# Performance work log

Hardware: AMD Instinct MI355X
Metric: run time of the kernel (lower is better)

## Reference

```python
import jax, jax.numpy as jnp
import numpy as np


def _normalize(x, axis=-1, eps=1e-12):
    n = jnp.linalg.norm(x, axis=axis, keepdims=True)
    return x / jnp.maximum(n, eps)


def _mlp(x, w1, b1, w2, b2):
    return jnp.maximum(x @ w1 + b1, 0.0) @ w2 + b2


def _quat_mul(a, b):
    # openfold (w, x, y, z) convention, Hamilton product
    aw, ax, ay, az = a[..., 0], a[..., 1], a[..., 2], a[..., 3]
    bw, bx, by, bz = b[..., 0], b[..., 1], b[..., 2], b[..., 3]
    return jnp.stack([
        aw * bw - ax * bx - ay * by - az * bz,
        aw * bx + ax * bw + ay * bz - az * by,
        aw * by - ax * bz + ay * bw + az * bx,
        aw * bz + ax * by - ay * bx + az * bw], axis=-1)


def _quat_rotate(q, v):
    # rotate vector v by unit quaternion q
    w = q[..., :1]
    u = q[..., 1:]
    t = 2.0 * jnp.cross(u, v)
    return v + w * t + jnp.cross(u, t)


def _conj(q):
    return q * jnp.asarray([1.0, -1.0, -1.0, -1.0], dtype=q.dtype)


def setup_inputs() -> dict:
    B, N, P, H, E, M = 2, 384, 128, 64, 32, 64
    key = jax.random.key(0)
    ks = iter(jax.random.split(key, 64))

    def nrm(shape):
        return jax.random.normal(next(ks), shape, dtype=jnp.float32)

    inp = {
        "frames_q": _normalize(nrm((B, N, 4))),
        "frames_x": nrm((B, N, 3)),
        "torsions": nrm((B, N, 7, 2)),
        "h": nrm((B, N, H)),
        "e": nrm((B, N, N, E)),
        "node_mask": jnp.ones((B, N), dtype=bool),
        "pocket_h": nrm((B, P, H)),
        "pocket_e": nrm((B, N, P, E)),
        "pocket_q": _normalize(nrm((B, P, 4))),
        "pocket_x": nrm((B, P, 3)),
        "pocket_mask": jnp.ones((B, P), dtype=bool),
    }
    # 2-layer MLPs with transition_size = 64
    for name, (fin, fout) in {"msg": (2 * H + E + 9, M), "feat": (H + M, H),
                              "tr": (M, 3), "qu": (M, 4), "to": (M, 14)}.items():
        inp[f"{name}_w1"] = nrm((fin, 64)) / np.sqrt(fin)
        inp[f"{name}_b1"] = nrm((64,)) * 0.01
        inp[f"{name}_w2"] = nrm((64, fout)) / np.sqrt(64)
        inp[f"{name}_b2"] = nrm((fout,)) * 0.01
    return inp


def reference(frames_q, frames_x, torsions, h, e, node_mask, pocket_h, pocket_e,
              pocket_q, pocket_x, pocket_mask,
              msg_w1, msg_b1, msg_w2, msg_b2,
              feat_w1, feat_b1, feat_w2, feat_b2,
              tr_w1, tr_b1, tr_w2, tr_b2,
              qu_w1, qu_b1, qu_w2, qu_b2,
              to_w1, to_b1, to_w2, to_b2):
    B, N, Hd = h.shape
    P = pocket_h.shape[-2]

    q_all = jnp.concatenate([frames_q, pocket_q], axis=-2)  # [B, N+P, 4]
    x_all = jnp.concatenate([frames_x, pocket_x], axis=-2)  # [B, N+P, 3]

    eye = jnp.eye(N, dtype=bool)
    mm = jnp.concatenate([
        node_mask[:, :, None] & node_mask[:, None, :] & ~eye,
        node_mask[:, :, None] & pocket_mask[:, None, :]], axis=-1)  # [B, N, N+P]

    vec = frames_x[:, :, None, :] - x_all[:, None, :, :]  # [B, N, N+P, 3]
    d2 = jnp.sum(vec * vec, axis=-1)                       # [B, N, N+P]
    qdot = jnp.abs(jnp.sum(frames_q[:, :, None, :] * q_all[:, None, :, :], axis=-1))

    # global -> local frame of node j applied to node i: R_j^T (x_i - t_j)
    qc = _conj(q_all)[:, None, :, :]                       # [B, 1, N+P, 4]
    local_x = _quat_rotate(qc, vec)                        # [B, N, N+P, 3]
    local_q = _quat_mul(qc, jnp.broadcast_to(frames_q[:, :, None, :], (B, N, N + P, 4)))

    feat = jnp.concatenate([
        jnp.broadcast_to(h[:, :, None, :], (B, N, N + P, Hd)),
        jnp.broadcast_to(jnp.concatenate([h, pocket_h], axis=-2)[:, None, :, :], (B, N, N + P, Hd)),
        jnp.concatenate([e, pocket_e], axis=-2),
        local_x, local_q, d2[..., None], qdot[..., None]], axis=-1)

    m = _mlp(feat, msg_w1, msg_b1, msg_w2, msg_b2) * mm[..., None]  # [B, N, N+P, M]
    msum = jnp.sum(m, axis=-2)                                      # [B, N, M]

    o = _mlp(jnp.concatenate([h, msum], axis=-1), feat_w1, feat_b1, feat_w2, feat_b2)

    dx = _mlp(m, tr_w1, tr_b1, tr_w2, tr_b2) * mm[..., None]        # [B, N, N+P, 3]

    ident = jnp.asarray([1.0, 0.0, 0.0, 0.0], dtype=frames_q.dtype)
    dq = _mlp(msum, qu_w1, qu_b1, qu_w2, qu_b2)
    dq = _normalize(jnp.where(node_mask[..., None], dq, ident))
    upd_q = _quat_mul(frames_q, dq)
    upd_q = _normalize(jnp.where(node_mask[..., None], upd_q, ident))

    qn_all = _normalize(q_all)
    gdx = jnp.sum(_quat_rotate(qn_all[:, None, :, :], dx), axis=-2)  # [B, N, 3]
    n_nb = (node_mask.sum(-1) + pocket_mask.sum(-1) - 1).astype(frames_x.dtype)
    upd_x = frames_x + gdx / n_nb[:, None, None]

    upd_torsions = _normalize(_mlp(msum, to_w1, to_b1, to_w2, to_b2).reshape(torsions.shape))

    return upd_q, upd_x, upd_torsions, o
```

## Files before the change

### kernel.cpp

```cpp
#include <hip/hip_runtime.h>
#include <math.h>

#define BB 2
#define NN 384
#define PP 128
#define HH 64
#define EE 32
#define NP 512
#define K1S 136
#define K2S 72

#define X_OFF (BB*NN*4)
#define T_OFF (X_OFF + BB*NN*3)
#define O_OFF (T_OFF + BB*NN*14)

using bf16x8 = __attribute__((ext_vector_type(8))) __bf16;
using f32x4  = __attribute__((ext_vector_type(4))) float;

__device__ __forceinline__ f32x4 MFMA(bf16x8 a, bf16x8 b, f32x4 c) {
  return __builtin_amdgcn_mfma_f32_16x16x32_bf16(a, b, c, 0, 0, 0);
}
__device__ __forceinline__ bf16x8 LDF(const __bf16* base, int off) {
  return *(const bf16x8*)(base + off);
}
__device__ __forceinline__ bf16x8 pack8(f32x4 lo, f32x4 hi) {
  bf16x8 r;
  r[0]=(__bf16)lo[0]; r[1]=(__bf16)lo[1]; r[2]=(__bf16)lo[2]; r[3]=(__bf16)lo[3];
  r[4]=(__bf16)hi[0]; r[5]=(__bf16)hi[1]; r[6]=(__bf16)hi[2]; r[7]=(__bf16)hi[3];
  return r;
}
__device__ __forceinline__ bf16x8 pack8v(float4 lo, float4 hi) {
  bf16x8 r;
  r[0]=(__bf16)lo.x; r[1]=(__bf16)lo.y; r[2]=(__bf16)lo.z; r[3]=(__bf16)lo.w;
  r[4]=(__bf16)hi.x; r[5]=(__bf16)hi.y; r[6]=(__bf16)hi.z; r[7]=(__bf16)hi.w;
  return r;
}
__device__ __forceinline__ int rowpos(int n) {
  const int t = (n>>5)*2 + ((n>>2)&1);
  const int q = ((n>>3)&3)*4 + (n&3);
  return t*16 + q;
}

__global__ __launch_bounds__(512, 2) void egnn_edge_swapped(
    const float* __restrict__ frames_q, const float* __restrict__ frames_x,
    const float* __restrict__ h, const float* __restrict__ e,
    const int* __restrict__ node_mask,
    const float* __restrict__ pocket_h, const float* __restrict__ pe,
    const float* __restrict__ pocket_q, const float* __restrict__ pocket_x,
    const int* __restrict__ pocket_mask,
    const float* __restrict__ w1, const float* __restrict__ b1,
    const float* __restrict__ w2, const float* __restrict__ b2,
    const float* __restrict__ tw1, const float* __restrict__ tb1,
    const float* __restrict__ tw2, const float* __restrict__ tb2,
    float* __restrict__ msum_ws, float* __restrict__ gdx_ws)
{
  __shared__ __align__(16) __bf16 s_w1p[64*K1S];
  __shared__ __align__(16) __bf16 s_w2p[64*K2S];
  __shared__ __align__(16) __bf16 s_tw1p[64*K2S];
  __shared__ __align__(16) __bf16 s_tw2p[16*K2S];
  __shared__ __align__(16) __bf16 s_geo[NP*16 + 8];
  __shared__ __align__(16) float s_qn[NP*4];
  __shared__ float s_maskf[NP];
  __shared__ __align__(16) float s_b2[64], s_tb1[64];
  __shared__ float s_tb2[4];
  __shared__ float s_msum[64], s_gdx[3];

  const int tid = threadIdx.x;
  const int b = blockIdx.x / NN, i = blockIdx.x % NN;

  for (int idx = tid; idx < 64*128; idx += 512) {
    const int n = idx & 63, k = idx >> 6;
    float v = 0.f;
    if      (k < 64)  v = w1[(64 + k)*64 + n];
    else if (k < 96)  v = w1[(128 + (k-64))*64 + n];
    else if (k < 105) v = w1[(160 + (k-96))*64 + n];
    if (k != 105) s_w1p[rowpos(n)*K1S + k] = (__bf16)v;
  }
  for (int idx = tid; idx < 64*64; idx += 512) {
    const int n = idx & 63, k = idx >> 6;
    s_w2p[rowpos(n)*K2S + k]  = (__bf16)w2[k*64 + n];
    s_tw1p[rowpos(n)*K2S + k] = (__bf16)tw1[k*64 + n];
  }
  for (int idx = tid; idx < 16*64; idx += 512) {
    const int row = idx >> 6, k = idx & 63;
    s_tw2p[row*K2S + k] = (__bf16)((row < 3) ? tw2[k*3 + row] : 0.f);
  }
  if (tid < 64) { s_b2[tid] = b2[tid]; s_tb1[tid] = tb1[tid]; s_msum[tid] = 0.f; }
  if (tid < 8)  s_geo[NP*16 + tid] = (__bf16)0.f;
  if (tid < 3)  { s_tb2[tid] = tb2[tid]; s_gdx[tid] = 0.f; }

  {
    const int n = tid >> 3, part = tid & 7;
    const float* hi = &h[(b*NN + i)*HH];
    float a = 0.f;
#pragma unroll
    for (int c = 0; c < 8; ++c) a = fmaf(hi[part*8 + c], w1[(part*8 + c)*64 + n], a);
    a += __shfl_xor(a, 1); a += __shfl_xor(a, 2); a += __shfl_xor(a, 4);
    if (part == 0) s_w1p[rowpos(n)*K1S + 105] = (__bf16)(a + b1[n]);
  }

  {
    const int j = tid;
    const int maski = node_mask[b*NN + i];
    const float qi0 = frames_q[(b*NN+i)*4+0], qi1 = frames_q[(b*NN+i)*4+1],
                qi2 = frames_q[(b*NN+i)*4+2], qi3 = frames_q[(b*NN+i)*4+3];
    const float xi0 = frames_x[(b*NN+i)*3+0], xi1 = frames_x[(b*NN+i)*3+1],
                xi2 = frames_x[(b*NN+i)*3+2];
    float qj0,qj1,qj2,qj3, xj0,xj1,xj2; int mj;
    if (j < NN) {
      const float4 q4 = *(const float4*)&frames_q[(b*NN+j)*4];
      qj0=q4.x; qj1=q4.y; qj2=q4.z; qj3=q4.w;
      xj0=frames_x[(b*NN+j)*3+0]; xj1=frames_x[(b*NN+j)*3+1]; xj2=frames_x[(b*NN+j)*3+2];
      mj = (node_mask[b*NN+j] != 0) && (j != i);
    } else {
      const int jp = j - NN;
      const float4 q4 = *(const float4*)&pocket_q[(b*PP+jp)*4];
      qj0=q4.x; qj1=q4.y; qj2=q4.z; qj3=q4.w;
      xj0=pocket_x[(b*PP+jp)*3+0]; xj1=pocket_x[(b*PP+jp)*3+1]; xj2=pocket_x[(b*PP+jp)*3+2];
      mj = (pocket_mask[b*PP+jp] != 0);
    }
    const float v0 = xi0 - xj0, v1 = xi1 - xj1, v2 = xi2 - xj2;
    const float d2 = v0*v0 + v1*v1 + v2*v2;
    const float qdot = fabsf(qi0*qj0 + qi1*qj1 + qi2*qj2 + qi3*qj3);
    const float cw = qj0, cx = -qj1, cy = -qj2, cz = -qj3;
    const float t0 = 2.f*(cy*v2 - cz*v1);
    const float t1 = 2.f*(cz*v0 - cx*v2);
    const float t2 = 2.f*(cx*v1 - cy*v0);
    const float lx0 = v0 + cw*t0 + (cy*t2 - cz*t1);
    const float lx1 = v1 + cw*t1 + (cz*t0 - cx*t2);
    const float lx2 = v2 + cw*t2 + (cx*t1 - cy*t0);
    const float lq0 = cw*qi0 - cx*qi1 - cy*qi2 - cz*qi3;
    const float lq1 = cw*qi1 + cx*qi0 + cy*qi3 - cz*qi2;
    const float lq2 = cw*qi2 - cx*qi3 + cy*qi0 + cz*qi1;
    const float lq3 = cw*qi3 + cx*qi2 - cy*qi1 + cz*qi0;
    __bf16* g = &s_geo[j*16];
    g[0]=(__bf16)lx0; g[1]=(__bf16)lx1; g[2]=(__bf16)lx2; g[3]=(__bf16)lq0;
    g[4]=(__bf16)lq1; g[5]=(__bf16)lq2; g[6]=(__bf16)lq3; g[7]=(__bf16)d2;
    g[8]=(__bf16)qdot; g[9]=(__bf16)1.f;
    g[10]=(__bf16)0.f; g[11]=(__bf16)0.f; g[12]=(__bf16)0.f;
    g[13]=(__bf16)0.f; g[14]=(__bf16)0.f; g[15]=(__bf16)0.f;
    s_maskf[j] = (maski && mj) ? 1.f : 0.f;
    const float inv = 1.f / fmaxf(sqrtf(qj0*qj0 + qj1*qj1 + qj2*qj2 + qj3*qj3), 1e-12f);
    float4* qn = (float4*)&s_qn[j*4];
    *qn = make_float4(qj0*inv, qj1*inv, qj2*inv, qj3*inv);
  }
  __syncthreads();

  const int wv = tid >> 6, lane = tid & 63;
  const int l15 = lane & 15, lg = lane >> 4;

  bf16x8 tw2f[2];
  tw2f[0] = *(const bf16x8*)&s_tw2p[l15*K2S +  0 + lg*8];
  tw2f[1] = *(const bf16x8*)&s_tw2p[l15*K2S + 32 + lg*8];
  const float tb2r0 = s_tb2[0], tb2r1 = s_tb2[1], tb2r2 = s_tb2[2];

  float msacc[16];
#pragma unroll
  for (int v = 0; v < 16; ++v) msacc[v] = 0.f;
  float gx0 = 0.f, gx1 = 0.f, gx2 = 0.f;

  const int o1base = l15*K1S + lg*8;
  const int o2base = l15*K2S + lg*8;
  const int obbase = lg*8;

#define LOADSTRIP(JB0, H0_,H1_,H2_,H3_,E0_,E1_) do {                        \
    const int jb_ = (JB0);                                                  \
    const int j_ = jb_ + l15;                                               \
    const float *hj_, *ej_;                                                 \
    if (jb_ < NN) {                                                         \
      hj_ = &h[(b*NN + j_)*HH];                                             \
      ej_ = &e[((b*NN + i)*NN + j_)*EE];                                    \
    } else {                                                                \
      const int jp_ = j_ - NN;                                              \
      hj_ = &pocket_h[(b*PP + jp_)*HH];                                     \
      ej_ = &pe[((b*NN + i)*PP + jp_)*EE];                                  \
    }                                                                       \
    H0_ = *(const float4*)&hj_[lg*8];                                       \
    H1_ = *(const float4*)&hj_[lg*8 + 4];                                   \
    H2_ = *(const float4*)&hj_[32 + lg*8];                                  \
    H3_ = *(const float4*)&hj_[32 + lg*8 + 4];                              \
    E0_ = *(const float4*)&ej_[lg*8];                                       \
    E1_ = *(const float4*)&ej_[lg*8 + 4];                                   \
  } while (0)

#pragma unroll
  for (int ss = 0; ss < 2; ++ss) {
    int o1 = o1base; asm volatile("" : "+v"(o1));
    int o2 = o2base; asm volatile("" : "+v"(o2));
    int ob = obbase; asm volatile("" : "+v"(ob));

    const int jbA = wv*64 + ss*32;
    const int jbB = jbA + 16;
    const int jA = jbA + l15, jB = jbB + l15;

    float4 hA0,hA1,hA2,hA3,eA0,eA1, hB0,hB1,hB2,hB3,eB0,eB1;
    LOADSTRIP(jbA, hA0,hA1,hA2,hA3,eA0,eA1);
    LOADSTRIP(jbB, hB0,hB1,hB2,hB3,eB0,eB1);
    const float maskA = s_maskf[jA];
    const float maskB = s_maskf[jB];

    const bf16x8 bfA0 = pack8v(hA0, hA1);
    const bf16x8 bfA1 = pack8v(hA2, hA3);
    const bf16x8 bfA2 = pack8v(eA0, eA1);
    const bf16x8 bfA3 = *(const bf16x8*)&s_geo[(lg < 2) ? (jA*16 + lg*8) : NP*16];
    const bf16x8 bfB0 = pack8v(hB0, hB1);
    const bf16x8 bfB1 = pack8v(hB2, hB3);
    const bf16x8 bfB2 = pack8v(eB0, eB1);
    const bf16x8 bfB3 = *(const bf16x8*)&s_geo[(lg < 2) ? (jB*16 + lg*8) : NP*16];

    const f32x4 zero4 = {0.f, 0.f, 0.f, 0.f};

    bf16x8 hbA0, hbA1, hbB0, hbB1;
    {
      f32x4 aA0, aA1, aB0, aB1;
      {
        const bf16x8 F0 = LDF(s_w1p, o1 + 0*16*K1S +  0);
        const bf16x8 F1 = LDF(s_w1p, o1 + 0*16*K1S + 32);
        const bf16x8 F2 = LDF(s_w1p, o1 + 0*16*K1S + 64);
        const bf16x8 F3 = LDF(s_w1p, o1 + 0*16*K1S + 96);
        aA0 = MFMA(F0,bfA0,zero4); aA0 = MFMA(F1,bfA1,aA0); aA0 = MFMA(F2,bfA2,aA0); aA0 = MFMA(F3,bfA3,aA0);
        aB0 = MFMA(F0,bfB0,zero4); aB0 = MFMA(F1,bfB1,aB0); aB0 = MFMA(F2,bfB2,aB0); aB0 = MFMA(F3,bfB3,aB0);
      }
      {
        const bf16x8 F0 = LDF(s_w1p, o1 + 1*16*K1S +  0);
        const bf16x8 F1 = LDF(s_w1p, o1 + 1*16*K1S + 32);
        const bf16x8 F2 = LDF(s_w1p, o1 + 1*16*K1S + 64);
        const bf16x8 F3 = LDF(s_w1p, o1 + 1*16*K1S + 96);
        aA1 = MFMA(F0,bfA0,zero4); aA1 = MFMA(F1,bfA1,aA1); aA1 = MFMA(F2,bfA2,aA1); aA1 = MFMA(F3,bfA3,aA1);
        aB1 = MFMA(F0,bfB0,zero4); aB1 = MFMA(F1,bfB1,aB1); aB1 = MFMA(F2,bfB2,aB1); aB1 = MFMA(F3,bfB3,aB1);
      }
#pragma unroll
      for (int r = 0; r < 4; ++r) {
        aA0[r] = fmaxf(aA0[r], 0.f); aA1[r] = fmaxf(aA1[r], 0.f);
        aB0[r] = fmaxf(aB0[r], 0.f); aB1[r] = fmaxf(aB1[r], 0.f);
      }
      hbA0 = pack8(aA0, aA1); hbB0 = pack8(aB0, aB1);
      {
        const bf16x8 F0 = LDF(s_w1p, o1 + 2*16*K1S +  0);
        const bf16x8 F1 = LDF(s_w1p, o1 + 2*16*K1S + 32);
        const bf16x8 F2 = LDF(s_w1p, o1 + 2*16*K1S + 64);
        const bf16x8 F3 = LDF(s_w1p, o1 + 2*16*K1S + 96);
        aA0 = MFMA(F0,bfA0,zero4); aA0 = MFMA(F1,bfA1,aA0); aA0 = MFMA(F2,bfA2,aA0); aA0 = MFMA(F3,bfA3,aA0);
        aB0 = MFMA(F0,bfB0,zero4); aB0 = MFMA(F1,bfB1,aB0); aB0 = MFMA(F2,bfB2,aB0); aB0 = MFMA(F3,bfB3,aB0);
      }
      {
        const bf16x8 F0 = LDF(s_w1p, o1 + 3*16*K1S +  0);
        const bf16x8 F1 = LDF(s_w1p, o1 + 3*16*K1S + 32);
        const bf16x8 F2 = LDF(s_w1p, o1 + 3*16*K1S + 64);
        const bf16x8 F3 = LDF(s_w1p, o1 + 3*16*K1S + 96);
        aA1 = MFMA(F0,bfA0,zero4); aA1 = MFMA(F1,bfA1,aA1); aA1 = MFMA(F2,bfA2,aA1); aA1 = MFMA(F3,bfA3,aA1);
        aB1 = MFMA(F0,bfB0,zero4); aB1 = MFMA(F1,bfB1,aB1); aB1 = MFMA(F2,bfB2,aB1); aB1 = MFMA(F3,bfB3,aB1);
      }
#pragma unroll
      for (int r = 0; r < 4; ++r) {
        aA0[r] = fmaxf(aA0[r], 0.f); aA1[r] = fmaxf(aA1[r], 0.f);
        aB0[r] = fmaxf(aB0[r], 0.f); aB1[r] = fmaxf(aB1[r], 0.f);
      }
      hbA1 = pack8(aA0, aA1); hbB1 = pack8(aB0, aB1);
    }

    bf16x8 mbA0, mbA1, mbB0, mbB1;
    {
      f32x4 cA0, cA1, cB0, cB1;
      {
        const bf16x8 F0 = LDF(s_w2p, o2 + 0*16*K2S +  0);
        const bf16x8 F1 = LDF(s_w2p, o2 + 0*16*K2S + 32);
        cA0 = MFMA(F0,hbA0,zero4); cA0 = MFMA(F1,hbA1,cA0);
        cB0 = MFMA(F0,hbB0,zero4); cB0 = MFMA(F1,hbB1,cB0);
      }
      {
        const bf16x8 F0 = LDF(s_w2p, o2 + 1*16*K2S +  0);
        const bf16x8 F1 = LDF(s_w2p, o2 + 1*16*K2S + 32);
        cA1 = MFMA(F0,hbA0,zero4); cA1 = MFMA(F1,hbA1,cA1);
        cB1 = MFMA(F0,hbB0,zero4); cB1 = MFMA(F1,hbB1,cB1);
      }
      const f32x4 bb0 = *(const f32x4*)&s_b2[ob + 0];
      const f32x4 bb1 = *(const f32x4*)&s_b2[ob + 4];
#pragma unroll
      for (int r = 0; r < 4; ++r) {
        cA0[r] = (cA0[r] + bb0[r]) * maskA;  cB0[r] = (cB0[r] + bb0[r]) * maskB;
        cA1[r] = (cA1[r] + bb1[r]) * maskA;  cB1[r] = (cB1[r] + bb1[r]) * maskB;
        msacc[0*4+r] += cA0[r] + cB0[r];
        msacc[1*4+r] += cA1[r] + cB1[r];
      }
      mbA0 = pack8(cA0, cA1); mbB0 = pack8(cB0, cB1);
      {
        const bf16x8 F0 = LDF(s_w2p, o2 + 2*16*K2S +  0);
        const bf16x8 F1 = LDF(s_w2p, o2 + 2*16*K2S + 32);
        cA0 = MFMA(F0,hbA0,zero4); cA0 = MFMA(F1,hbA1,cA0);
        cB0 = MFMA(F0,hbB0,zero4); cB0 = MFMA(F1,hbB1,cB0);
      }
      {
        const bf16x8 F0 = LDF(s_w2p, o2 + 3*16*K2S +  0);
        const bf16x8 F1 = LDF(s_w2p, o2 + 3*16*K2S + 32);
        cA1 = MFMA(F0,hbA0,zero4); cA1 = MFMA(F1,hbA1,cA1);
        cB1 = MFMA(F0,hbB0,zero4); cB1 = MFMA(F1,hbB1,cB1);
      }
      const f32x4 bb2 = *(const f32x4*)&s_b2[ob + 32];
      const f32x4 bb3 = *(const f32x4*)&s_b2[ob + 36];
#pragma unroll
      for (int r = 0; r < 4; ++r) {
        cA0[r] = (cA0[r] + bb2[r]) * maskA;  cB0[r] = (cB0[r] + bb2[r]) * maskB;
        cA1[r] = (cA1[r] + bb3[r]) * maskA;  cB1[r] = (cB1[r] + bb3[r]) * maskB;
        msacc[2*4+r] += cA0[r] + cB0[r];
        msacc[3*4+r] += cA1[r] + cB1[r];
      }
      mbA1 = pack8(cA0, cA1); mbB1 = pack8(cB0, cB1);
    }

    bf16x8 thbA0, thbA1, thbB0, thbB1;
    {
      f32x4 dA0, dA1, dB0, dB1;
      {
        const bf16x8 F0 = LDF(s_tw1p, o2 + 0*16*K2S +  0);
        const bf16x8 F1 = LDF(s_tw1p, o2 + 0*16*K2S + 32);
        dA0 = MFMA(F0,mbA0,zero4); dA0 = MFMA(F1,mbA1,dA0);
        dB0 = MFMA(F0,mbB0,zero4); dB0 = MFMA(F1,mbB1,dB0);
      }
      {
        const bf16x8 F0 = LDF(s_tw1p, o2 + 1*16*K2S +  0);
        const bf16x8 F1 = LDF(s_tw1p, o2 + 1*16*K2S + 32);
        dA1 = MFMA(F0,mbA0,zero4); dA1 = MFMA(F1,mbA1,dA1);
        dB1 = MFMA(F0,mbB0,zero4); dB1 = MFMA(F1,mbB1,dB1);
      }
      {
        const f32x4 tb0 = *(const f32x4*)&s_tb1[ob + 0];
        const f32x4 tb1v = *(const f32x4*)&s_tb1[ob + 4];
#pragma unroll
        for (int r = 0; r < 4; ++r) {
          dA0[r] = fmaxf(dA0[r] + tb0[r], 0.f);  dB0[r] = fmaxf(dB0[r] + tb0[r], 0.f);
          dA1[r] = fmaxf(dA1[r] + tb1v[r], 0.f); dB1[r] = fmaxf(dB1[r] + tb1v[r], 0.f);
        }
      }
      thbA0 = pack8(dA0, dA1); thbB0 = pack8(dB0, dB1);
      {
        const bf16x8 F0 = LDF(s_tw1p, o2 + 2*16*K2S +  0);
        const bf16x8 F1 = LDF(s_tw1p, o2 + 2*16*K2S + 32);
        dA0 = MFMA(F0,mbA0,zero4); dA0 = MFMA(F1,mbA1,dA0);
        dB0 = MFMA(F0,mbB0,zero4); dB0 = MFMA(F1,mbB1,dB0);
      }
      {
        const bf16x8 F0 = LDF(s_tw1p, o2 + 3*16*K2S +  0);
        const bf16x8 F1 = LDF(s_tw1p, o2 + 3*16*K2S + 32);
        dA1 = MFMA(F0,mbA0,zero4); dA1 = MFMA(F1,mbA1,dA1);
        dB1 = MFMA(F0,mbB0,zero4); dB1 = MFMA(F1,mbB1,dB1);
      }
      {
        const f32x4 tb2v = *(const f32x4*)&s_tb1[ob + 32];
        const f32x4 tb3v = *(const f32x4*)&s_tb1[ob + 36];
#pragma unroll
        for (int r = 0; r < 4; ++r) {
          dA0[r] = fmaxf(dA0[r] + tb2v[r], 0.f);  dB0[r] = fmaxf(dB0[r] + tb2v[r], 0.f);
          dA1[r] = fmaxf(dA1[r] + tb3v[r], 0.f);  dB1[r] = fmaxf(dB1[r] + tb3v[r], 0.f);
        }
      }
      thbA1 = pack8(dA0, dA1); thbB1 = pack8(dB0, dB1);
    }

    f32x4 daccA = MFMA(tw2f[0], thbA0, zero4);
    daccA = MFMA(tw2f[1], thbA1, daccA);
    f32x4 daccB = MFMA(tw2f[0], thbB0, zero4);
    daccB = MFMA(tw2f[1], thbB1, daccB);

    if (lg == 0) {
      {
        const float dx0 = (daccA[0] + tb2r0) * maskA;
        const float dx1 = (daccA[1] + tb2r1) * maskA;
        const float dx2 = (daccA[2] + tb2r2) * maskA;
        const float4 qn = *(const float4*)&s_qn[jA*4];
        const float w = qn.x, ux = qn.y, uy = qn.z, uz = qn.w;
        const float r0 = 2.f*(uy*dx2 - uz*dx1);
        const float r1 = 2.f*(uz*dx0 - ux*dx2);
        const float r2 = 2.f*(ux*dx1 - uy*dx0);
        gx0 += dx0 + w*r0 + (uy*r2 - uz*r1);
        gx1 += dx1 + w*r1 + (uz*r0 - ux*r2);
        gx2 += dx2 + w*r2 + (ux*r1 - uy*r0);
      }
      {
        const float dx0 = (daccB[0] + tb2r0) * maskB;
        const float dx1 = (daccB[1] + tb2r1) * maskB;
        const float dx2 = (daccB[2] + tb2r2) * maskB;
        const float4 qn = *(const float4*)&s_qn[jB*4];
        const float w = qn.x, ux = qn.y, uy = qn.z, uz = qn.w;
        const float r0 = 2.f*(uy*dx2 - uz*dx1);
        const float r1 = 2.f*(uz*dx0 - ux*dx2);
        const float r2 = 2.f*(ux*dx1 - uy*dx0);
        gx0 += dx0 + w*r0 + (uy*r2 - uz*r1);
        gx1 += dx1 + w*r1 + (uz*r0 - ux*r2);
        gx2 += dx2 + w*r2 + (ux*r1 - uy*r0);
      }
    }
  }
#undef LOADSTRIP

#pragma unroll
  for (int v = 0; v < 16; ++v) {
    float x = msacc[v];
    x += __shfl_xor(x, 1); x += __shfl_xor(x, 2);
    x += __shfl_xor(x, 4); x += __shfl_xor(x, 8);
    if (l15 == 0) {
      const int n2 = (v>>3)*32 + lg*8 + ((v>>2)&1)*4 + (v&3);
      atomicAdd(&s_msum[n2], x);
    }
  }
  {
    float v0 = (lg == 0) ? gx0 : 0.f;
    float v1 = (lg == 0) ? gx1 : 0.f;
    float v2 = (lg == 0) ? gx2 : 0.f;
#pragma unroll
    for (int sft = 1; sft < 64; sft <<= 1) {
      v0 += __shfl_xor(v0, sft); v1 += __shfl_xor(v1, sft); v2 += __shfl_xor(v2, sft);
    }
    if (lane == 0) { atomicAdd(&s_gdx[0], v0); atomicAdd(&s_gdx[1], v1); atomicAdd(&s_gdx[2], v2); }
  }
  __syncthreads();
  if (tid < 64) msum_ws[(b*NN + i)*64 + tid] = s_msum[tid];
  if (tid >= 64 && tid < 67) gdx_ws[(b*NN + i)*3 + (tid - 64)] = s_gdx[tid - 64];
}

__global__ __launch_bounds__(64) void egnn_node_kernel(
    const float* __restrict__ frames_q, const float* __restrict__ frames_x,
    const float* __restrict__ h,
    const int* __restrict__ node_mask, const int* __restrict__ pocket_mask,
    const float* __restrict__ fw1, const float* __restrict__ fb1,
    const float* __restrict__ fw2, const float* __restrict__ fb2,
    const float* __restrict__ qw1, const float* __restrict__ qb1,
    const float* __restrict__ qw2, const float* __restrict__ qb2,
    const float* __restrict__ tow1, const float* __restrict__ tob1,
    const float* __restrict__ tow2, const float* __restrict__ tob2,
    const float* __restrict__ msum_ws, const float* __restrict__ gdx_ws,
    float* __restrict__ out)
{
  const int t  = threadIdx.x;
  const int bi = blockIdx.x;
  const int b = bi / NN, i = bi % NN;
  __shared__ float s_h[64], s_ms[64], s_hid[64], s_tmp[16];

  s_h[t]  = h[(b*NN+i)*HH + t];
  s_ms[t] = msum_ws[(b*NN+i)*64 + t];

  int cnt = 0;
  for (int k = t; k < NN; k += 64) cnt += (node_mask[b*NN+k] != 0);
  for (int k = t; k < PP; k += 64) cnt += (pocket_mask[b*PP+k] != 0);
  cnt += __shfl_xor(cnt,1); cnt += __shfl_xor(cnt,2); cnt += __shfl_xor(cnt,4);
  cnt += __shfl_xor(cnt,8); cnt += __shfl_xor(cnt,16); cnt += __shfl_xor(cnt,32);
  const float n_nb = (float)(cnt - 1);

  __syncthreads();
  float a = fb1[t];
  for (int k = 0; k < 64; ++k) a = fmaf(s_h[k],  fw1[k*64 + t], a);
  for (int k = 0; k < 64; ++k) a = fmaf(s_ms[k], fw1[(64+k)*64 + t], a);
  s_hid[t] = fmaxf(a, 0.f);
  __syncthreads();
  float ov = fb2[t];
  for (int k = 0; k < 64; ++k) ov = fmaf(s_hid[k], fw2[k*64 + t], ov);
  out[O_OFF + (b*NN+i)*64 + t] = ov;

  __syncthreads();
  float aq = qb1[t];
  for (int k = 0; k < 64; ++k) aq = fmaf(s_ms[k], qw1[k*64 + t], aq);
  s_hid[t] = fmaxf(aq, 0.f);
  __syncthreads();
  if (t < 4) {
    float d = qb2[t];
    for (int k = 0; k < 64; ++k) d = fmaf(s_hid[k], qw2[k*4 + t], d);
    s_tmp[t] = d;
  }
  __syncthreads();
  if (t == 0) {
    const int mi = node_mask[b*NN+i];
    float d0,d1,d2,d3;
    if (mi) { d0=s_tmp[0]; d1=s_tmp[1]; d2=s_tmp[2]; d3=s_tmp[3]; }
    else    { d0=1.f; d1=0.f; d2=0.f; d3=0.f; }
    float nrm = fmaxf(sqrtf(d0*d0+d1*d1+d2*d2+d3*d3), 1e-12f);
    d0/=nrm; d1/=nrm; d2/=nrm; d3/=nrm;
    const float q0=frames_q[(b*NN+i)*4+0], q1=frames_q[(b*NN+i)*4+1],
                q2=frames_q[(b*NN+i)*4+2], q3=frames_q[(b*NN+i)*4+3];
    float u0 = q0*d0 - q1*d1 - q2*d2 - q3*d3;
    float u1 = q0*d1 + q1*d0 + q2*d3 - q3*d2;
    float u2 = q0*d2 - q1*d3 + q2*d0 + q3*d1;
    float u3 = q0*d3 + q1*d2 - q2*d1 + q3*d0;
    if (!mi) { u0=1.f; u1=0.f; u2=0.f; u3=0.f; }
    float nrm2 = fmaxf(sqrtf(u0*u0+u1*u1+u2*u2+u3*u3), 1e-12f);
    out[(b*NN+i)*4+0]=u0/nrm2; out[(b*NN+i)*4+1]=u1/nrm2;
    out[(b*NN+i)*4+2]=u2/nrm2; out[(b*NN+i)*4+3]=u3/nrm2;
  }
  if (t < 3) {
    out[X_OFF + (b*NN+i)*3 + t] = frames_x[(b*NN+i)*3+t] + gdx_ws[(b*NN+i)*3+t] / n_nb;
  }

  __syncthreads();
  float at = tob1[t];
  for (int k = 0; k < 64; ++k) at = fmaf(s_ms[k], tow1[k*64 + t], at);
  s_hid[t] = fmaxf(at, 0.f);
  __syncthreads();
  if (t < 14) {
    float v = tob2[t];
    for (int k = 0; k < 64; ++k) v = fmaf(s_hid[k], tow2[k*14 + t], v);
    s_tmp[t] = v;
  }
  __syncthreads();
  if (t < 14) {
    const int p = t & ~1;
    const float a0 = s_tmp[p], a1 = s_tmp[p+1];
    const float nrm = fmaxf(sqrtf(a0*a0 + a1*a1), 1e-12f);
    out[T_OFF + (b*NN+i)*14 + t] = s_tmp[t] / nrm;
  }
}

extern "C" void kernel_launch(void* const* d_in, const int* in_sizes, int n_in,
                              void* d_out, int out_size, void* d_ws, size_t ws_size,
                              hipStream_t stream) {
  const float* frames_q    = (const float*)d_in[0];
  const float* frames_x    = (const float*)d_in[1];
  const float* h           = (const float*)d_in[3];
  const float* e           = (const float*)d_in[4];
  const int*   node_mask   = (const int*)d_in[5];
  const float* pocket_h    = (const float*)d_in[6];
  const float* pocket_e    = (const float*)d_in[7];
  const float* pocket_q    = (const float*)d_in[8];
  const float* pocket_x    = (const float*)d_in[9];
  const int*   pocket_mask = (const int*)d_in[10];
  const float* msg_w1 = (const float*)d_in[11];
  const float* msg_b1 = (const float*)d_in[12];
  const float* msg_w2 = (const float*)d_in[13];
  const float* msg_b2 = (const float*)d_in[14];
  const float* feat_w1 = (const float*)d_in[15];
  const float* feat_b1 = (const float*)d_in[16];
  const float* feat_w2 = (const float*)d_in[17];
  const float* feat_b2 = (const float*)d_in[18];
  const float* tr_w1 = (const float*)d_in[19];
  const float* tr_b1 = (const float*)d_in[20];
  const float* tr_w2 = (const float*)d_in[21];
  const float* tr_b2 = (const float*)d_in[22];
  const float* qu_w1 = (const float*)d_in[23];
  const float* qu_b1 = (const float*)d_in[24];
  const float* qu_w2 = (const float*)d_in[25];
  const float* qu_b2 = (const float*)d_in[26];
  const float* to_w1 = (const float*)d_in[27];
  const float* to_b1 = (const float*)d_in[28];
  const float* to_w2 = (const float*)d_in[29];
  const float* to_b2 = (const float*)d_in[30];

  float* out = (float*)d_out;
  float* msum_ws = (float*)d_ws;
  float* gdx_ws  = msum_ws + BB*NN*64;

  egnn_edge_swapped<<<dim3(BB*NN), dim3(512), 0, stream>>>(
      frames_q, frames_x, h, e, node_mask,
      pocket_h, pocket_e, pocket_q, pocket_x, pocket_mask,
      msg_w1, msg_b1, msg_w2, msg_b2,
      tr_w1, tr_b1, tr_w2, tr_b2,
      msum_ws, gdx_ws);

  egnn_node_kernel<<<dim3(BB*NN), dim3(64), 0, stream>>>(
      frames_q, frames_x, h, node_mask, pocket_mask,
      feat_w1, feat_b1, feat_w2, feat_b2,
      qu_w1, qu_b1, qu_w2, qu_b2,
      to_w1, to_b1, to_w2, to_b2,
      msum_ws, gdx_ws, out);
}
```

Before: 65.02 us.

## Precompute h_j @ W1 per neighbor in a pre-kernel to shrink edge GEMM K

Adds a small kernel that computes the neighbor-feature part of the first message-MLP layer (h_j times its W1 slice) once per node into a workspace. The edge kernel then seeds its MFMA accumulators with these fp32 partial products and only multiplies the edge-feature and geometry slices, which cuts K from 128 to 64. This removes redundant per-edge recomputation and halves the first-layer MFMA work and the W1 shared-memory footprint. In exchange it adds a kernel launch and reads a 64-float fp32 row per neighbor instead of the raw h row.

```diff
diff --git a/kernel.cpp b/kernel.cpp
--- a/kernel.cpp
+++ b/kernel.cpp
@@ -7,7 +7,7 @@
 #define HH 64
 #define EE 32
 #define NP 512
-#define K1S 136
+#define K1S 72
 #define K2S 72
 
 #define X_OFF (BB*NN*4)
@@ -35,10 +35,30 @@
   r[4]=(__bf16)hi.x; r[5]=(__bf16)hi.y; r[6]=(__bf16)hi.z; r[7]=(__bf16)hi.w;
   return r;
 }
+__device__ __forceinline__ f32x4 f4(float4 v) {
+  f32x4 r; r[0]=v.x; r[1]=v.y; r[2]=v.z; r[3]=v.w; return r;
+}
 __device__ __forceinline__ int rowpos(int n) {
   const int t = (n>>5)*2 + ((n>>2)&1);
   const int q = ((n>>3)&3)*4 + (n&3);
   return t*16 + q;
+}
+
+__global__ __launch_bounds__(256) void egnn_hpre(
+    const float* __restrict__ h, const float* __restrict__ pocket_h,
+    const float* __restrict__ w1, float* __restrict__ Hws)
+{
+  const int g = threadIdx.x >> 6, n = threadIdx.x & 63;
+  const int row = blockIdx.x*4 + g;
+  const int b = row >> 9, j = row & (NP-1);
+  const float* src = (j < NN) ? &h[(b*NN + j)*HH] : &pocket_h[(b*PP + (j - NN))*HH];
+  __shared__ float s_r[4][64];
+  s_r[g][n] = src[n];
+  __syncthreads();
+  float a = 0.f;
+#pragma unroll 8
+  for (int k = 0; k < 64; ++k) a = fmaf(s_r[g][k], w1[(64 + k)*64 + n], a);
+  Hws[row*64 + n] = a;
 }
 
 __global__ __launch_bounds__(512, 2) void egnn_edge_swapped(
@@ -52,6 +72,7 @@
     const float* __restrict__ w2, const float* __restrict__ b2,
     const float* __restrict__ tw1, const float* __restrict__ tb1,
     const float* __restrict__ tw2, const float* __restrict__ tb2,
+    const float* __restrict__ Hws,
     float* __restrict__ msum_ws, float* __restrict__ gdx_ws)
 {
   __shared__ __align__(16) __bf16 s_w1p[64*K1S];
@@ -68,13 +89,13 @@
   const int tid = threadIdx.x;
   const int b = blockIdx.x / NN, i = blockIdx.x % NN;
 
-  for (int idx = tid; idx < 64*128; idx += 512) {
+  for (int idx = tid; idx < 64*64; idx += 512) {
     const int n = idx & 63, k = idx >> 6;
     float v = 0.f;
-    if      (k < 64)  v = w1[(64 + k)*64 + n];
-    else if (k < 96)  v = w1[(128 + (k-64))*64 + n];
-    else if (k < 105) v = w1[(160 + (k-96))*64 + n];
-    if (k != 105) s_w1p[rowpos(n)*K1S + k] = (__bf16)v;
+    if      (k < 32) v = w1[(128 + k)*64 + n];
+    else if (k < 40) v = w1[(160 + (k-32))*64 + n];
+    else if (k == 40) v = w1[168*64 + n];
+    if (k != 41) s_w1p[rowpos(n)*K1S + k] = (__bf16)v;
   }
   for (int idx = tid; idx < 64*64; idx += 512) {
     const int n = idx & 63, k = idx >> 6;
@@ -96,7 +117,7 @@
 #pragma unroll
     for (int c = 0; c < 8; ++c) a = fmaf(hi[part*8 + c], w1[(part*8 + c)*64 + n], a);
     a += __shfl_xor(a, 1); a += __shfl_xor(a, 2); a += __shfl_xor(a, 4);
-    if (part == 0) s_w1p[rowpos(n)*K1S + 105] = (__bf16)(a + b1[n]);
+    if (part == 0) s_w1p[rowpos(n)*K1S + 41] = (__bf16)(a + b1[n]);
   }
 
   {
@@ -163,26 +184,6 @@
   const int o2base = l15*K2S + lg*8;
   const int obbase = lg*8;
 
-#define LOADSTRIP(JB0, H0_,H1_,H2_,H3_,E0_,E1_) do {                        \
-    const int jb_ = (JB0);                                                  \
-    const int j_ = jb_ + l15;                                               \
-    const float *hj_, *ej_;                                                 \
-    if (jb_ < NN) {                                                         \
-      hj_ = &h[(b*NN + j_)*HH];                                             \
-      ej_ = &e[((b*NN + i)*NN + j_)*EE];                                    \
-    } else {                                                                \
-      const int jp_ = j_ - NN;                                              \
-      hj_ = &pocket_h[(b*PP + jp_)*HH];                                     \
-      ej_ = &pe[((b*NN + i)*PP + jp_)*EE];                                  \
-    }                                                                       \
-    H0_ = *(const float4*)&hj_[lg*8];                                       \
-    H1_ = *(const float4*)&hj_[lg*8 + 4];                                   \
-    H2_ = *(const float4*)&hj_[32 + lg*8];                                  \
-    H3_ = *(const float4*)&hj_[32 + lg*8 + 4];                              \
-    E0_ = *(const float4*)&ej_[lg*8];                                       \
-    E1_ = *(const float4*)&ej_[lg*8 + 4];                                   \
-  } while (0)
-
 #pragma unroll
   for (int ss = 0; ss < 2; ++ss) {
     int o1 = o1base; asm volatile("" : "+v"(o1));
@@ -193,18 +194,30 @@
     const int jbB = jbA + 16;
     const int jA = jbA + l15, jB = jbB + l15;
 
-    float4 hA0,hA1,hA2,hA3,eA0,eA1, hB0,hB1,hB2,hB3,eB0,eB1;
-    LOADSTRIP(jbA, hA0,hA1,hA2,hA3,eA0,eA1);
-    LOADSTRIP(jbB, hB0,hB1,hB2,hB3,eB0,eB1);
+    const float* ejA = (jbA < NN) ? &e[((b*NN + i)*NN + jA)*EE]
+                                  : &pe[((b*NN + i)*PP + (jA - NN))*EE];
+    const float* ejB = (jbB < NN) ? &e[((b*NN + i)*NN + jB)*EE]
+                                  : &pe[((b*NN + i)*PP + (jB - NN))*EE];
+    const float4 eA0 = *(const float4*)&ejA[lg*8];
+    const float4 eA1 = *(const float4*)&ejA[lg*8 + 4];
+    const float4 eB0 = *(const float4*)&ejB[lg*8];
+    const float4 eB1 = *(const float4*)&ejB[lg*8 + 4];
+    const float* HA = &Hws[(b*NP + jA)*64];
+    const float* HB = &Hws[(b*NP + jB)*64];
+    const float4 iA0 = *(const float4*)&HA[lg*8];
+    const float4 iA1 = *(const float4*)&HA[lg*8 + 4];
+    const float4 iA2 = *(const float4*)&HA[32 + lg*8];
+    const float4 iA3 = *(const float4*)&HA[32 + lg*8 + 4];
+    const float4 iB0 = *(const float4*)&HB[lg*8];
+    const float4 iB1 = *(const float4*)&HB[lg*8 + 4];
+    const float4 iB2 = *(const float4*)&HB[32 + lg*8];
+    const float4 iB3 = *(const float4*)&HB[32 + lg*8 + 4];
+
     const float maskA = s_maskf[jA];
     const float maskB = s_maskf[jB];
 
-    const bf16x8 bfA0 = pack8v(hA0, hA1);
-    const bf16x8 bfA1 = pack8v(hA2, hA3);
     const bf16x8 bfA2 = pack8v(eA0, eA1);
     const bf16x8 bfA3 = *(const bf16x8*)&s_geo[(lg < 2) ? (jA*16 + lg*8) : NP*16];
-    const bf16x8 bfB0 = pack8v(hB0, hB1);
-    const bf16x8 bfB1 = pack8v(hB2, hB3);
     const bf16x8 bfB2 = pack8v(eB0, eB1);
     const bf16x8 bfB3 = *(const bf16x8*)&s_geo[(lg < 2) ? (jB*16 + lg*8) : NP*16];
 
@@ -212,22 +225,18 @@
 
     bf16x8 hbA0, hbA1, hbB0, hbB1;
     {
-      f32x4 aA0, aA1, aB0, aB1;
+      f32x4 aA0 = f4(iA0), aA1 = f4(iA1), aB0 = f4(iB0), aB1 = f4(iB1);
       {
         const bf16x8 F0 = LDF(s_w1p, o1 + 0*16*K1S +  0);
         const bf16x8 F1 = LDF(s_w1p, o1 + 0*16*K1S + 32);
-        const bf16x8 F2 = LDF(s_w1p, o1 + 0*16*K1S + 64);
-        const bf16x8 F3 = LDF(s_w1p, o1 + 0*16*K1S + 96);
-        aA0 = MFMA(F0,bfA0,zero4); aA0 = MFMA(F1,bfA1,aA0); aA0 = MFMA(F2,bfA2,aA0); aA0 = MFMA(F3,bfA3,aA0);
-        aB0 = MFMA(F0,bfB0,zero4); aB0 = MFMA(F1,bfB1,aB0); aB0 = MFMA(F2,bfB2,aB0); aB0 = MFMA(F3,bfB3,aB0);
+        aA0 = MFMA(F0,bfA2,aA0); aA0 = MFMA(F1,bfA3,aA0);
+        aB0 = MFMA(F0,bfB2,aB0); aB0 = MFMA(F1,bfB3,aB0);
       }
       {
         const bf16x8 F0 = LDF(s_w1p, o1 + 1*16*K1S +  0);
         const bf16x8 F1 = LDF(s_w1p, o1 + 1*16*K1S + 32);
-        const bf16x8 F2 = LDF(s_w1p, o1 + 1*16*K1S + 64);
-        const bf16x8 F3 = LDF(s_w1p, o1 + 1*16*K1S + 96);
-        aA1 = MFMA(F0,bfA0,zero4); aA1 = MFMA(F1,bfA1,aA1); aA1 = MFMA(F2,bfA2,aA1); aA1 = MFMA(F3,bfA3,aA1);
-        aB1 = MFMA(F0,bfB0,zero4); aB1 = MFMA(F1,bfB1,aB1); aB1 = MFMA(F2,bfB2,aB1); aB1 = MFMA(F3,bfB3,aB1);
+        aA1 = MFMA(F0,bfA2,aA1); aA1 = MFMA(F1,bfA3,aA1);
+        aB1 = MFMA(F0,bfB2,aB1); aB1 = MFMA(F1,bfB3,aB1);
       }
 #pragma unroll
       for (int r = 0; r < 4; ++r) {
@@ -235,28 +244,25 @@
         aB0[r] = fmaxf(aB0[r], 0.f); aB1[r] = fmaxf(aB1[r], 0.f);
       }
       hbA0 = pack8(aA0, aA1); hbB0 = pack8(aB0, aB1);
+      f32x4 aA2 = f4(iA2), aA3 = f4(iA3), aB2 = f4(iB2), aB3 = f4(iB3);
       {
         const bf16x8 F0 = LDF(s_w1p, o1 + 2*16*K1S +  0);
         const bf16x8 F1 = LDF(s_w1p, o1 + 2*16*K1S + 32);
-        const bf16x8 F2 = LDF(s_w1p, o1 + 2*16*K1S + 64);
-        const bf16x8 F3 = LDF(s_w1p, o1 + 2*16*K1S + 96);
-        aA0 = MFMA(F0,bfA0,zero4); aA0 = MFMA(F1,bfA1,aA0); aA0 = MFMA(F2,bfA2,aA0); aA0 = MFMA(F3,bfA3,aA0);
-        aB0 = MFMA(F0,bfB0,zero4); aB0 = MFMA(F1,bfB1,aB0); aB0 = MFMA(F2,bfB2,aB0); aB0 = MFMA(F3,bfB3,aB0);
+        aA2 = MFMA(F0,bfA2,aA2); aA2 = MFMA(F1,bfA3,aA2);
+        aB2 = MFMA(F0,bfB2,aB2); aB2 = MFMA(F1,bfB3,aB2);
       }
       {
         const bf16x8 F0 = LDF(s_w1p, o1 + 3*16*K1S +  0);
         const bf16x8 F1 = LDF(s_w1p, o1 + 3*16*K1S + 32);
-        const bf16x8 F2 = LDF(s_w1p, o1 + 3*16*K1S + 64);
-        const bf16x8 F3 = LDF(s_w1p, o1 + 3*16*K1S + 96);
-        aA1 = MFMA(F0,bfA0,zero4); aA1 = MFMA(F1,bfA1,aA1); aA1 = MFMA(F2,bfA2,aA1); aA1 = MFMA(F3,bfA3,aA1);
-        aB1 = MFMA(F0,bfB0,zero4); aB1 = MFMA(F1,bfB1,aB1); aB1 = MFMA(F2,bfB2,aB1); aB1 = MFMA(F3,bfB3,aB1);
+        aA3 = MFMA(F0,bfA2,aA3); aA3 = MFMA(F1,bfA3,aA3);
+        aB3 = MFMA(F0,bfB2,aB3); aB3 = MFMA(F1,bfB3,aB3);
       }
 #pragma unroll
       for (int r = 0; r < 4; ++r) {
-        aA0[r] = fmaxf(aA0[r], 0.f); aA1[r] = fmaxf(aA1[r], 0.f);
-        aB0[r] = fmaxf(aB0[r], 0.f); aB1[r] = fmaxf(aB1[r], 0.f);
-      }
-      hbA1 = pack8(aA0, aA1); hbB1 = pack8(aB0, aB1);
+        aA2[r] = fmaxf(aA2[r], 0.f); aA3[r] = fmaxf(aA3[r], 0.f);
+        aB2[r] = fmaxf(aB2[r], 0.f); aB3[r] = fmaxf(aB3[r], 0.f);
+      }
+      hbA1 = pack8(aA2, aA3); hbB1 = pack8(aB2, aB3);
     }
 
     bf16x8 mbA0, mbA1, mbB0, mbB1;
@@ -391,7 +397,6 @@
       }
     }
   }
-#undef LOADSTRIP
 
 #pragma unroll
   for (int v = 0; v < 16; ++v) {
@@ -545,13 +550,16 @@
   float* out = (float*)d_out;
   float* msum_ws = (float*)d_ws;
   float* gdx_ws  = msum_ws + BB*NN*64;
+  float* Hws     = gdx_ws + BB*NN*3;
+
+  egnn_hpre<<<dim3(BB*NP/4), dim3(256), 0, stream>>>(h, pocket_h, msg_w1, Hws);
 
   egnn_edge_swapped<<<dim3(BB*NN), dim3(512), 0, stream>>>(
       frames_q, frames_x, h, e, node_mask,
       pocket_h, pocket_e, pocket_q, pocket_x, pocket_mask,
       msg_w1, msg_b1, msg_w2, msg_b2,
       tr_w1, tr_b1, tr_w2, tr_b2,
-      msum_ws, gdx_ws);
+      Hws, msum_ws, gdx_ws);
 
   egnn_node_kernel<<<dim3(BB*NN), dim3(64), 0, stream>>>(
       frames_q, frames_x, h, node_mask, pocket_mask,
```

Measured after the change: 68.42 us. 5.2% more time.

## Fuse node-update MLPs into edge kernel and drop the second launch

Applied to the files above, without the earlier changes.

Moves the per-node feature, quaternion and torsion MLPs into the tail of the edge kernel so each block finishes its node directly from shared msum/gdx, removing the workspace round-trip and the second kernel launch. The neighbour count now comes from a ballot of the masks already loaded in the geometry phase, with per-wave popcounts, instead of a separate reduction loop. The three first-layer matvecs are split across all 512 threads with shuffle reductions. In exchange the tail adds serial work and extra shared memory to a 512-thread block that may limit occupancy.

```diff
diff --git a/kernel.cpp b/kernel.cpp
--- a/kernel.cpp
+++ b/kernel.cpp
@@ -41,7 +41,7 @@
   return t*16 + q;
 }
 
-__global__ __launch_bounds__(512, 2) void egnn_edge_swapped(
+__global__ __launch_bounds__(512, 2) void egnn_fused(
     const float* __restrict__ frames_q, const float* __restrict__ frames_x,
     const float* __restrict__ h, const float* __restrict__ e,
     const int* __restrict__ node_mask,
@@ -52,7 +52,13 @@
     const float* __restrict__ w2, const float* __restrict__ b2,
     const float* __restrict__ tw1, const float* __restrict__ tb1,
     const float* __restrict__ tw2, const float* __restrict__ tb2,
-    float* __restrict__ msum_ws, float* __restrict__ gdx_ws)
+    const float* __restrict__ fw1, const float* __restrict__ fb1,
+    const float* __restrict__ fw2, const float* __restrict__ fb2,
+    const float* __restrict__ qw1, const float* __restrict__ qb1,
+    const float* __restrict__ qw2, const float* __restrict__ qb2,
+    const float* __restrict__ tow1, const float* __restrict__ tob1,
+    const float* __restrict__ tow2, const float* __restrict__ tob2,
+    float* __restrict__ out)
 {
   __shared__ __align__(16) __bf16 s_w1p[64*K1S];
   __shared__ __align__(16) __bf16 s_w2p[64*K2S];
@@ -64,6 +70,10 @@
   __shared__ __align__(16) float s_b2[64], s_tb1[64];
   __shared__ float s_tb2[4];
   __shared__ float s_msum[64], s_gdx[3];
+  __shared__ float s_hi[64];
+  __shared__ float s_hido[64], s_hidq[64], s_hidt[64];
+  __shared__ float s_tmpq[4], s_tmpt[14];
+  __shared__ int   s_wcnt[8];
 
   const int tid = threadIdx.x;
   const int b = blockIdx.x / NN, i = blockIdx.x % NN;
@@ -85,7 +95,10 @@
     const int row = idx >> 6, k = idx & 63;
     s_tw2p[row*K2S + k] = (__bf16)((row < 3) ? tw2[k*3 + row] : 0.f);
   }
-  if (tid < 64) { s_b2[tid] = b2[tid]; s_tb1[tid] = tb1[tid]; s_msum[tid] = 0.f; }
+  if (tid < 64) {
+    s_b2[tid] = b2[tid]; s_tb1[tid] = tb1[tid]; s_msum[tid] = 0.f;
+    s_hi[tid] = h[(b*NN + i)*HH + tid];
+  }
   if (tid < 8)  s_geo[NP*16 + tid] = (__bf16)0.f;
   if (tid < 3)  { s_tb2[tid] = tb2[tid]; s_gdx[tid] = 0.f; }
 
@@ -106,18 +119,24 @@
                 qi2 = frames_q[(b*NN+i)*4+2], qi3 = frames_q[(b*NN+i)*4+3];
     const float xi0 = frames_x[(b*NN+i)*3+0], xi1 = frames_x[(b*NN+i)*3+1],
                 xi2 = frames_x[(b*NN+i)*3+2];
-    float qj0,qj1,qj2,qj3, xj0,xj1,xj2; int mj;
+    float qj0,qj1,qj2,qj3, xj0,xj1,xj2; int mj, raw;
     if (j < NN) {
       const float4 q4 = *(const float4*)&frames_q[(b*NN+j)*4];
       qj0=q4.x; qj1=q4.y; qj2=q4.z; qj3=q4.w;
       xj0=frames_x[(b*NN+j)*3+0]; xj1=frames_x[(b*NN+j)*3+1]; xj2=frames_x[(b*NN+j)*3+2];
-      mj = (node_mask[b*NN+j] != 0) && (j != i);
+      raw = (node_mask[b*NN+j] != 0);
+      mj  = raw && (j != i);
     } else {
       const int jp = j - NN;
       const float4 q4 = *(const float4*)&pocket_q[(b*PP+jp)*4];
       qj0=q4.x; qj1=q4.y; qj2=q4.z; qj3=q4.w;
       xj0=pocket_x[(b*PP+jp)*3+0]; xj1=pocket_x[(b*PP+jp)*3+1]; xj2=pocket_x[(b*PP+jp)*3+2];
-      mj = (pocket_mask[b*PP+jp] != 0);
+      raw = (pocket_mask[b*PP+jp] != 0);
+      mj  = raw;
+    }
+    {
+      const unsigned long long bal = __ballot(raw);
+      if ((tid & 63) == 0) s_wcnt[tid >> 6] = __popcll(bal);
     }
     const float v0 = xi0 - xj0, v1 = xi1 - xj1, v2 = xi2 - xj2;
     const float d2 = v0*v0 + v1*v1 + v2*v2;
@@ -414,63 +433,61 @@
     if (lane == 0) { atomicAdd(&s_gdx[0], v0); atomicAdd(&s_gdx[1], v1); atomicAdd(&s_gdx[2], v2); }
   }
   __syncthreads();
-  if (tid < 64) msum_ws[(b*NN + i)*64 + tid] = s_msum[tid];
-  if (tid >= 64 && tid < 67) gdx_ws[(b*NN + i)*3 + (tid - 64)] = s_gdx[tid - 64];
-}
-
-__global__ __launch_bounds__(64) void egnn_node_kernel(
-    const float* __restrict__ frames_q, const float* __restrict__ frames_x,
-    const float* __restrict__ h,
-    const int* __restrict__ node_mask, const int* __restrict__ pocket_mask,
-    const float* __restrict__ fw1, const float* __restrict__ fb1,
-    const float* __restrict__ fw2, const float* __restrict__ fb2,
-    const float* __restrict__ qw1, const float* __restrict__ qb1,
-    const float* __restrict__ qw2, const float* __restrict__ qb2,
-    const float* __restrict__ tow1, const float* __restrict__ tob1,
-    const float* __restrict__ tow2, const float* __restrict__ tob2,
-    const float* __restrict__ msum_ws, const float* __restrict__ gdx_ws,
-    float* __restrict__ out)
-{
-  const int t  = threadIdx.x;
-  const int bi = blockIdx.x;
-  const int b = bi / NN, i = bi % NN;
-  __shared__ float s_h[64], s_ms[64], s_hid[64], s_tmp[16];
-
-  s_h[t]  = h[(b*NN+i)*HH + t];
-  s_ms[t] = msum_ws[(b*NN+i)*64 + t];
-
-  int cnt = 0;
-  for (int k = t; k < NN; k += 64) cnt += (node_mask[b*NN+k] != 0);
-  for (int k = t; k < PP; k += 64) cnt += (pocket_mask[b*PP+k] != 0);
-  cnt += __shfl_xor(cnt,1); cnt += __shfl_xor(cnt,2); cnt += __shfl_xor(cnt,4);
-  cnt += __shfl_xor(cnt,8); cnt += __shfl_xor(cnt,16); cnt += __shfl_xor(cnt,32);
-  const float n_nb = (float)(cnt - 1);
-
+
+  {
+    const int n = tid >> 3, part = tid & 7;
+    float ao = 0.f, aq = 0.f, at = 0.f;
+#pragma unroll
+    for (int c = 0; c < 16; ++c) {
+      const int kk = part*16 + c;
+      const float x = (kk < 64) ? s_hi[kk] : s_msum[kk - 64];
+      ao = fmaf(x, fw1[kk*64 + n], ao);
+    }
+#pragma unroll
+    for (int c = 0; c < 8; ++c) {
+      const int kk = part*8 + c;
+      aq = fmaf(s_msum[kk], qw1[kk*64 + n], aq);
+      at = fmaf(s_msum[kk], tow1[kk*64 + n], at);
+    }
+    ao += __shfl_xor(ao,1); ao += __shfl_xor(ao,2); ao += __shfl_xor(ao,4);
+    aq += __shfl_xor(aq,1); aq += __shfl_xor(aq,2); aq += __shfl_xor(aq,4);
+    at += __shfl_xor(at,1); at += __shfl_xor(at,2); at += __shfl_xor(at,4);
+    if (part == 0) {
+      s_hido[n] = fmaxf(ao + fb1[n], 0.f);
+      s_hidq[n] = fmaxf(aq + qb1[n], 0.f);
+      s_hidt[n] = fmaxf(at + tob1[n], 0.f);
+    }
+  }
   __syncthreads();
-  float a = fb1[t];
-  for (int k = 0; k < 64; ++k) a = fmaf(s_h[k],  fw1[k*64 + t], a);
-  for (int k = 0; k < 64; ++k) a = fmaf(s_ms[k], fw1[(64+k)*64 + t], a);
-  s_hid[t] = fmaxf(a, 0.f);
+  {
+    const int n = tid >> 3, part = tid & 7;
+    float ov = 0.f;
+#pragma unroll
+    for (int c = 0; c < 8; ++c) {
+      const int kk = part*8 + c;
+      ov = fmaf(s_hido[kk], fw2[kk*64 + n], ov);
+    }
+    ov += __shfl_xor(ov,1); ov += __shfl_xor(ov,2); ov += __shfl_xor(ov,4);
+    if (part == 0) out[O_OFF + (b*NN+i)*64 + n] = ov + fb2[n];
+  }
+  if (tid < 4) {
+    float d = qb2[tid];
+#pragma unroll 8
+    for (int k = 0; k < 64; ++k) d = fmaf(s_hidq[k], qw2[k*4 + tid], d);
+    s_tmpq[tid] = d;
+  }
+  if (tid >= 64 && tid < 78) {
+    const int t = tid - 64;
+    float v = tob2[t];
+#pragma unroll 8
+    for (int k = 0; k < 64; ++k) v = fmaf(s_hidt[k], tow2[k*14 + t], v);
+    s_tmpt[t] = v;
+  }
   __syncthreads();
-  float ov = fb2[t];
-  for (int k = 0; k < 64; ++k) ov = fmaf(s_hid[k], fw2[k*64 + t], ov);
-  out[O_OFF + (b*NN+i)*64 + t] = ov;
-
-  __syncthreads();
-  float aq = qb1[t];
-  for (int k = 0; k < 64; ++k) aq = fmaf(s_ms[k], qw1[k*64 + t], aq);
-  s_hid[t] = fmaxf(aq, 0.f);
-  __syncthreads();
-  if (t < 4) {
-    float d = qb2[t];
-    for (int k = 0; k < 64; ++k) d = fmaf(s_hid[k], qw2[k*4 + t], d);
-    s_tmp[t] = d;
-  }
-  __syncthreads();
-  if (t == 0) {
+  if (tid == 0) {
     const int mi = node_mask[b*NN+i];
     float d0,d1,d2,d3;
-    if (mi) { d0=s_tmp[0]; d1=s_tmp[1]; d2=s_tmp[2]; d3=s_tmp[3]; }
+    if (mi) { d0=s_tmpq[0]; d1=s_tmpq[1]; d2=s_tmpq[2]; d3=s_tmpq[3]; }
     else    { d0=1.f; d1=0.f; d2=0.f; d3=0.f; }
     float nrm = fmaxf(sqrtf(d0*d0+d1*d1+d2*d2+d3*d3), 1e-12f);
     d0/=nrm; d1/=nrm; d2/=nrm; d3/=nrm;
@@ -485,26 +502,19 @@
     out[(b*NN+i)*4+0]=u0/nrm2; out[(b*NN+i)*4+1]=u1/nrm2;
     out[(b*NN+i)*4+2]=u2/nrm2; out[(b*NN+i)*4+3]=u3/nrm2;
   }
-  if (t < 3) {
-    out[X_OFF + (b*NN+i)*3 + t] = frames_x[(b*NN+i)*3+t] + gdx_ws[(b*NN+i)*3+t] / n_nb;
-  }
-
-  __syncthreads();
-  float at = tob1[t];
-  for (int k = 0; k < 64; ++k) at = fmaf(s_ms[k], tow1[k*64 + t], at);
-  s_hid[t] = fmaxf(at, 0.f);
-  __syncthreads();
-  if (t < 14) {
-    float v = tob2[t];
-    for (int k = 0; k < 64; ++k) v = fmaf(s_hid[k], tow2[k*14 + t], v);
-    s_tmp[t] = v;
-  }
-  __syncthreads();
-  if (t < 14) {
+  if (tid >= 4 && tid < 7) {
+    const int t = tid - 4;
+    const int cnt = s_wcnt[0]+s_wcnt[1]+s_wcnt[2]+s_wcnt[3]
+                  + s_wcnt[4]+s_wcnt[5]+s_wcnt[6]+s_wcnt[7];
+    const float n_nb = (float)(cnt - 1);
+    out[X_OFF + (b*NN+i)*3 + t] = frames_x[(b*NN+i)*3 + t] + s_gdx[t] / n_nb;
+  }
+  if (tid >= 16 && tid < 30) {
+    const int t = tid - 16;
     const int p = t & ~1;
-    const float a0 = s_tmp[p], a1 = s_tmp[p+1];
+    const float a0 = s_tmpt[p], a1 = s_tmpt[p+1];
     const float nrm = fmaxf(sqrtf(a0*a0 + a1*a1), 1e-12f);
-    out[T_OFF + (b*NN+i)*14 + t] = s_tmp[t] / nrm;
+    out[T_OFF + (b*NN+i)*14 + t] = s_tmpt[t] / nrm;
   }
 }
 
@@ -543,20 +553,14 @@
   const float* to_b2 = (const float*)d_in[30];
 
   float* out = (float*)d_out;
-  float* msum_ws = (float*)d_ws;
-  float* gdx_ws  = msum_ws + BB*NN*64;
-
-  egnn_edge_swapped<<<dim3(BB*NN), dim3(512), 0, stream>>>(
+
+  egnn_fused<<<dim3(BB*NN), dim3(512), 0, stream>>>(
       frames_q, frames_x, h, e, node_mask,
       pocket_h, pocket_e, pocket_q, pocket_x, pocket_mask,
       msg_w1, msg_b1, msg_w2, msg_b2,
       tr_w1, tr_b1, tr_w2, tr_b2,
-      msum_ws, gdx_ws);
-
-  egnn_node_kernel<<<dim3(BB*NN), dim3(64), 0, stream>>>(
-      frames_q, frames_x, h, node_mask, pocket_mask,
       feat_w1, feat_b1, feat_w2, feat_b2,
       qu_w1, qu_b1, qu_w2, qu_b2,
       to_w1, to_b1, to_w2, to_b2,
-      msum_ws, gdx_ws, out);
-}
+      out);
+}
```

Measured after the change: 74.74 us. 14.9% more time.
